# Optimization experiments

Measured on AMD Instinct MI355X. Metric: run time of the kernel, lower is better.

## Reference

```python
import jax, jax.numpy as jnp
import numpy as np

BS, N, F_IN, H, F_OUT = 4, 2048, 128, 4, 64


def setup_inputs() -> dict:
    key = jax.random.key(0)
    k1, k2, k3, k4, k5 = jax.random.split(key, 5)
    x = jax.random.normal(k1, (BS, N, F_IN), dtype=jnp.float32)
    adj = jax.random.randint(k2, (BS, N, N), 0, 2).astype(bool)
    # guarantee self-loops so no softmax row is all -inf
    adj = jnp.logical_or(adj, jnp.eye(N, dtype=bool)[None])
    # xavier-uniform-ish scales
    w = jax.random.uniform(k3, (H, F_IN, F_OUT), dtype=jnp.float32,
                           minval=-1.0, maxval=1.0) * np.sqrt(6.0 / (F_IN + F_OUT))
    a_src = jax.random.uniform(k4, (H, F_OUT, 1), dtype=jnp.float32,
                               minval=-1.0, maxval=1.0) * np.sqrt(6.0 / (F_OUT + 1))
    a_dst = jax.random.uniform(k5, (H, F_OUT, 1), dtype=jnp.float32,
                               minval=-1.0, maxval=1.0) * np.sqrt(6.0 / (F_OUT + 1))
    bias = jnp.zeros((F_OUT,), dtype=jnp.float32)
    return {"x": x, "adj": adj, "w": w, "a_src": a_src, "a_dst": a_dst, "bias": bias}


def reference(x, adj, w, a_src, a_dst, bias):
    bs, n = x.shape[:2]
    # h_prime: [bs, H, n, F_OUT]
    h = jnp.einsum('bnf,hfo->bhno', x, w)
    th = jnp.tanh(h)
    s_src = jnp.einsum('bhno,ho->bhn', th, a_src[..., 0])  # [bs,H,n]
    s_dst = jnp.einsum('bhno,ho->bhn', th, a_dst[..., 0])  # [bs,H,n]
    # attn[b,h,i,j] = src[b,h,i] + dst[b,h,j]
    attn = s_src[..., :, None] + s_dst[..., None, :]
    attn = jnp.where(attn >= 0, attn, 0.2 * attn)  # leaky_relu(0.2)
    attn = jnp.where(adj[:, None], attn, -jnp.inf)  # mask = ~adj
    p = jax.nn.softmax(attn, axis=-1)  # dropout is identity at eval
    out = jnp.einsum('bhij,bhjo->bhio', p, h) + bias  # [bs,H,n,F_OUT]
    # torch .view(bs, n, -1) on contiguous [bs,H,n,F_OUT]: raw reshape
    return out.reshape(bs, n, -1)
```

## Files before the change

kernel.cpp:

```cpp
#include <hip/hip_runtime.h>
#include <hip/hip_fp16.h>

#define NN   2048
#define FIN  128
#define FOUT 64
#define LOG2E 1.44269504088896f

using f16x8 = __attribute__((ext_vector_type(8))) _Float16;
using f16x4 = __attribute__((ext_vector_type(4))) _Float16;
using f16x2 = __attribute__((ext_vector_type(2))) _Float16;
using f32x4 = __attribute__((ext_vector_type(4))) float;
using i32x4 = __attribute__((ext_vector_type(4))) int;

__device__ inline float fast_exp2(float x) {
#if __has_builtin(__builtin_amdgcn_exp2f)
    return __builtin_amdgcn_exp2f(x);
#else
    return exp2f(x);
#endif
}
__device__ inline float fast_rcp(float x) {
#if __has_builtin(__builtin_amdgcn_rcpf)
    return __builtin_amdgcn_rcpf(x);
#else
    return 1.0f / x;
#endif
}
__device__ inline float fast_tanh(float x) {
    float e = fast_exp2(2.0f * LOG2E * x);
    return 1.0f - 2.0f * fast_rcp(e + 1.0f);
}
__device__ inline unsigned cvt2h(float a, float b) {
    return __builtin_bit_cast(unsigned, __builtin_amdgcn_cvt_pkrtz(a, b));
}
__device__ inline f16x2 pkmax(f16x2 a, f16x2 b) {
#if __has_builtin(__builtin_elementwise_max)
    return __builtin_elementwise_max(a, b);
#else
    f16x2 r; r[0] = a[0] > b[0] ? a[0] : b[0]; r[1] = a[1] > b[1] ? a[1] : b[1];
    return r;
#endif
}
__device__ inline unsigned bmask(unsigned wb, int p) {
    unsigned lo = (unsigned)(-(int)((wb >> (2 * p)) & 1u));
    unsigned hi = (unsigned)(-(int)((wb >> (2 * p + 1)) & 1u));
    return (hi & 0xFFFF0000u) | (lo & 0x0000FFFFu);
}


__global__ __launch_bounds__(256) void k1_proj(
    const float* __restrict__ x, const float* __restrict__ w,
    const float* __restrict__ a_src, const float* __restrict__ a_dst,
    const int* __restrict__ adj,
    _Float16* __restrict__ h16B, float* __restrict__ ssrc, float* __restrict__ sdst,
    unsigned int* __restrict__ adjbits)
{
    __shared__ __align__(16) _Float16 xf[8192];
    __shared__ __align__(16) _Float16 wf[8192];

    const int t    = threadIdx.x;
    const int bx   = blockIdx.x;
    const int bh   = bx >> 5;
    const int tile = bx & 31;
    const int b    = bh >> 2;
    const int h    = bh & 3;
    const int n0   = tile * 64;
    const int wv   = t >> 6;
    const int lane = t & 63;
    const int m    = lane & 15;
    const int g    = lane >> 4;

    {
        const int o  = t & 63;
        const int kc = t >> 6;
        const float* wcol = w + h * FIN * FOUT + o;
        _Float16* dst = wf + ((kc * 4 + (o >> 4)) * 512) + (o & 15) * 8;
#pragma unroll
        for (int hi = 0; hi < 4; ++hi) {
            unsigned u0 = cvt2h(wcol[(kc * 32 + hi * 8 + 0) * FOUT],
                                wcol[(kc * 32 + hi * 8 + 1) * FOUT]);
            unsigned u1 = cvt2h(wcol[(kc * 32 + hi * 8 + 2) * FOUT],
                                wcol[(kc * 32 + hi * 8 + 3) * FOUT]);
            unsigned u2 = cvt2h(wcol[(kc * 32 + hi * 8 + 4) * FOUT],
                                wcol[(kc * 32 + hi * 8 + 5) * FOUT]);
            unsigned u3 = cvt2h(wcol[(kc * 32 + hi * 8 + 6) * FOUT],
                                wcol[(kc * 32 + hi * 8 + 7) * FOUT]);
            *(uint4*)(dst + hi * 128) = uint4{u0, u1, u2, u3};
        }
    }
    {
        const int r  = t >> 2;
        const int kc = t & 3;
        const float* xr = x + ((size_t)(b * NN + n0 + r)) * FIN + kc * 32;
        _Float16* dst = xf + ((r >> 4) * 16 + kc * 4) * 128 + (r & 15) * 8;
#pragma unroll
        for (int g2 = 0; g2 < 4; ++g2) {
            f32x4 va = *(const f32x4*)(xr + g2 * 8);
            f32x4 vb = *(const f32x4*)(xr + g2 * 8 + 4);
            *(uint4*)(dst + g2 * 128) = uint4{cvt2h(va[0], va[1]), cvt2h(va[2], va[3]),
                                              cvt2h(vb[0], vb[1]), cvt2h(vb[2], vb[3])};
        }
    }
    __syncthreads();

    const int rg = wv;
    f32x4 acc0 = {0,0,0,0}, acc1 = {0,0,0,0}, acc2 = {0,0,0,0}, acc3 = {0,0,0,0};
#pragma unroll
    for (int kc = 0; kc < 4; ++kc) {
        f16x8 av = *(const f16x8*)(xf + (rg * 16 + kc * 4 + g) * 128 + m * 8);
        const _Float16* wb_ = wf + kc * 4 * 512 + lane * 8;
        acc0 = __builtin_amdgcn_mfma_f32_16x16x32_f16(av, *(const f16x8*)(wb_), acc0, 0, 0, 0);
        acc1 = __builtin_amdgcn_mfma_f32_16x16x32_f16(av, *(const f16x8*)(wb_ + 512), acc1, 0, 0, 0);
        acc2 = __builtin_amdgcn_mfma_f32_16x16x32_f16(av, *(const f16x8*)(wb_ + 1024), acc2, 0, 0, 0);
        acc3 = __builtin_amdgcn_mfma_f32_16x16x32_f16(av, *(const f16x8*)(wb_ + 1536), acc3, 0, 0, 0);
    }

    float s1r[4] = {0,0,0,0}, s2r[4] = {0,0,0,0};
    const int jg = n0 + rg * 16 + g * 4;
#define PROC(accX, ot)  do {                                                    \
        float asv = a_src[h * FOUT + (ot) * 16 + m];                            \
        float adv = a_dst[h * FOUT + (ot) * 16 + m];                            \
        _Pragma("unroll")                                                       \
        for (int r = 0; r < 4; ++r) {                                           \
            float th = fast_tanh(accX[r]);                                      \
            s1r[r] += th * asv;                                                 \
            s2r[r] += th * adv;                                                 \
        }                                                                       \
        unsigned u0 = cvt2h(accX[0], accX[1]);                                  \
        unsigned u1 = cvt2h(accX[2], accX[3]);                                  \
        int off = bh * 131072 + (jg >> 5) * 2048 + (ot) * 512                   \
                + (((jg >> 3) & 3) * 16 + m) * 8 + (jg & 7);                    \
        *(uint2*)(h16B + off) = uint2{u0, u1};                                  \
    } while (0)
    PROC(acc0, 0); PROC(acc1, 1); PROC(acc2, 2); PROC(acc3, 3);
#undef PROC
#pragma unroll
    for (int msk = 1; msk <= 8; msk <<= 1) {
#pragma unroll
        for (int r = 0; r < 4; ++r) {
            s1r[r] += __shfl_xor(s1r[r], msk);
            s2r[r] += __shfl_xor(s2r[r], msk);
        }
    }
    if (m == 0) {
#pragma unroll
        for (int r = 0; r < 4; ++r) {
            ssrc[bh * NN + jg + r] = s1r[r] * LOG2E;
            sdst[bh * NN + jg + r] = s2r[r] * LOG2E;
        }
    }

    {
        const int  frow0 = bx * 16;
        const int* asrc  = adj + (size_t)frow0 * NN;
#pragma unroll
        for (int w4 = 0; w4 < 4; ++w4) {
            int widx  = t + 256 * w4;
            int row_l = widx >> 6;
            int wc    = widx & 63;
            const i32x4* p = (const i32x4*)(asrc + (size_t)row_l * NN + wc * 32);
            unsigned int wbits = 0;
#pragma unroll
            for (int k = 0; k < 8; ++k) {
                i32x4 v = p[k];
                wbits |= (unsigned int)(v[0] & 1) << (4 * k);
                wbits |= (unsigned int)(v[1] & 1) << (4 * k + 1);
                wbits |= (unsigned int)(v[2] & 1) << (4 * k + 2);
                wbits |= (unsigned int)(v[3] & 1) << (4 * k + 3);
            }
            adjbits[(size_t)(frow0 + row_l) * 64 + wc] = wbits;
        }
    }
}

__global__ __launch_bounds__(512, 6) void k2_attn(
    const unsigned int* __restrict__ adjbits,
    const _Float16* __restrict__ h16B,
    const float* __restrict__ ssrc, const float* __restrict__ sdst,
    const float* __restrict__ bias, float* __restrict__ out)
{
    __shared__ __align__(16) char smem[42016];
    _Float16*     Bf     = (_Float16*)smem;
    unsigned int* adjw   = (unsigned int*)(smem + 16384);
    _Float16*     E1h    = (_Float16*)(smem + 33792);
    _Float16*     E2h    = (_Float16*)(smem + 37888);
    float*        redmax = (float*)(smem + 41984);
    float*        comb   = (float*)smem;

    const int t    = threadIdx.x;
    const int wv   = t >> 6;
    const int lane = t & 63;
    const int bh   = blockIdx.x >> 5;
    const int i0   = (blockIdx.x & 31) << 6;
    const int b    = bh >> 2;
    const int rg   = wv >> 1;
    const int par  = wv & 1;
    const int m    = lane & 15;
    const int g    = lane >> 4;

    const _Float16* Bsrc = h16B + bh * 131072;

#define STAGE(bufi_, s_)                                                        \
    __builtin_amdgcn_global_load_lds(                                           \
        (const __attribute__((address_space(1))) unsigned int*)(Bsrc + (s_) * 4096 + t * 8), \
        (__attribute__((address_space(3))) unsigned int*)(Bf + (bufi_) * 4096 + t * 8), \
        16, 0, 0)

    STAGE(0, 0);
    {
        const uint4* asrc = (const uint4*)(adjbits + ((size_t)b * NN + i0) * 64);
#pragma unroll
        for (int k = 0; k < 2; ++k) {
            int idx = t + 512 * k;
            uint4 v = asrc[idx];
            *(uint4*)(adjw + (idx >> 4) * 68 + (idx & 15) * 4) = v;
        }
    }
    float dm;
    {
        f32x4 dv = *(const f32x4*)(sdst + bh * NN + t * 4);
        *(uint2*)(E1h + t * 4) = uint2{cvt2h(fast_exp2(dv[0]), fast_exp2(dv[1])),
                                       cvt2h(fast_exp2(dv[2]), fast_exp2(dv[3]))};
        *(uint2*)(E2h + t * 4) = uint2{cvt2h(fast_exp2(0.2f * dv[0]), fast_exp2(0.2f * dv[1])),
                                       cvt2h(fast_exp2(0.2f * dv[2]), fast_exp2(0.2f * dv[3]))};
        dm = fmaxf(fmaxf(dv[0], dv[1]), fmaxf(dv[2], dv[3]));
#pragma unroll
        for (int msk = 1; msk <= 32; msk <<= 1) dm = fmaxf(dm, __shfl_xor(dm, msk));
        if (lane == 0) redmax[wv] = dm;
    }
    asm volatile("s_waitcnt vmcnt(0)" ::: "memory");
    __syncthreads();

    float D = redmax[0];
#pragma unroll
    for (int k = 1; k < 8; ++k) D = fmaxf(D, redmax[k]);

    const int row = i0 + rg * 16 + m;
    const float sA = ssrc[bh * NN + row];
    float c = sA + D; c = fmaxf(c, 0.2f * c);
    const float K1f = fast_exp2(sA - c);
    const float K2f = fast_exp2(fmaf(0.2f, sA, -c));
    f16x2 K1h2; { _Float16 q = (_Float16)K1f; K1h2[0] = q; K1h2[1] = q; }
    f16x2 K2h2; { _Float16 q = (_Float16)K2f; K2h2[0] = q; K2h2[1] = q; }

    f32x4 acc0 = {0,0,0,0}, acc1 = {0,0,0,0}, acc2 = {0,0,0,0}, acc3 = {0,0,0,0};
    f32x4 accz = {0,0,0,0};
    f16x8 ones;
#pragma unroll
    for (int i = 0; i < 8; ++i) ones[i] = (_Float16)1.0f;

    const int arow68 = (rg * 16 + m) * 68;

#pragma unroll
    for (int s = 0; s < 32; ++s) {
        if (s < 31) {
            STAGE((s + 1) & 1, s + 1);
            asm volatile("s_waitcnt vmcnt(1)" ::: "memory");
        } else {
            asm volatile("s_waitcnt vmcnt(0)" ::: "memory");
        }
        __builtin_amdgcn_sched_barrier(0);
        __builtin_amdgcn_s_barrier();
        __builtin_amdgcn_sched_barrier(0);

        const int ci = 2 * s + par;
        unsigned wb = adjw[arow68 + ci] >> (8 * g);
        union { f16x8 v; f16x2 p[4]; unsigned u[4]; } E1u, E2u, af;
        E1u.v = *(const f16x8*)(E1h + ci * 32 + 8 * g);
        E2u.v = *(const f16x8*)(E2h + ci * 32 + 8 * g);

        const _Float16* bb = Bf + (s & 1) * 4096 + par * 2048 + lane * 8;
        f16x8 b0 = *(const f16x8*)(bb);
        f16x8 b1 = *(const f16x8*)(bb + 512);
        f16x8 b2 = *(const f16x8*)(bb + 1024);
        f16x8 b3 = *(const f16x8*)(bb + 1536);

#pragma unroll
        for (int p = 0; p < 4; ++p) {
            f16x2 v1 = K1h2 * E1u.p[p];
            f16x2 v2 = K2h2 * E2u.p[p];
            f16x2 vm = pkmax(v1, v2);
            af.u[p] = __builtin_bit_cast(unsigned, vm) & bmask(wb, p);
        }

        acc0 = __builtin_amdgcn_mfma_f32_16x16x32_f16(af.v, b0, acc0, 0, 0, 0);
        acc1 = __builtin_amdgcn_mfma_f32_16x16x32_f16(af.v, b1, acc1, 0, 0, 0);
        acc2 = __builtin_amdgcn_mfma_f32_16x16x32_f16(af.v, b2, acc2, 0, 0, 0);
        acc3 = __builtin_amdgcn_mfma_f32_16x16x32_f16(af.v, b3, acc3, 0, 0, 0);
        accz = __builtin_amdgcn_mfma_f32_16x16x32_f16(af.v, ones, accz, 0, 0, 0);

        __builtin_amdgcn_s_barrier();
    }
#undef STAGE

    __syncthreads();
    if (par == 1) {
        float* cp = comb + (rg * 64 + lane) * 20;
#pragma unroll
        for (int r = 0; r < 4; ++r) {
            cp[0 + r]  = acc0[r];
            cp[4 + r]  = acc1[r];
            cp[8 + r]  = acc2[r];
            cp[12 + r] = acc3[r];
            cp[16 + r] = accz[r];
        }
    }
    __syncthreads();
    if (par == 0) {
        const float* cp = comb + (rg * 64 + lane) * 20;
        float zs[4];
#pragma unroll
        for (int r = 0; r < 4; ++r) zs[r] = accz[r] + cp[16 + r];
        size_t obase = ((size_t)bh * NN + i0 + rg * 16) * FOUT;
#pragma unroll
        for (int ot = 0; ot < 4; ++ot) {
            float bv = bias[ot * 16 + m];
            f32x4 a = (ot == 0) ? acc0 : (ot == 1) ? acc1 : (ot == 2) ? acc2 : acc3;
#pragma unroll
            for (int r = 0; r < 4; ++r) {
                float v = (a[r] + cp[ot * 4 + r]) / zs[r] + bv;
                out[obase + (size_t)(g * 4 + r) * FOUT + ot * 16 + m] = v;
            }
        }
    }
}

extern "C" void kernel_launch(void* const* d_in, const int* in_sizes, int n_in,
                              void* d_out, int out_size, void* d_ws, size_t ws_size,
                              hipStream_t stream) {
    (void)in_sizes; (void)n_in; (void)out_size; (void)ws_size;
    const float* x     = (const float*)d_in[0];
    const int*   adj   = (const int*)d_in[1];
    const float* w     = (const float*)d_in[2];
    const float* a_src = (const float*)d_in[3];
    const float* a_dst = (const float*)d_in[4];
    const float* bias  = (const float*)d_in[5];
    float*       out   = (float*)d_out;

    _Float16*     h16B    = (_Float16*)d_ws;
    float*        ssrc    = (float*)((char*)d_ws + 4194304);
    float*        sdst    = (float*)((char*)d_ws + 4194304 + 131072);
    unsigned int* adjbits = (unsigned int*)((char*)d_ws + 4718592);

    k1_proj<<<512, 256, 0, stream>>>(x, w, a_src, a_dst, adj, h16B, ssrc, sdst, adjbits);
    k2_attn<<<512, 512, 0, stream>>>(adjbits, h16B, ssrc, sdst, bias, out);
}
```

Before: 41.31 us.

## Switch attention aggregation to 32x32x16 MFMA with 4-way key split

The attention kernel moves from 16x16x32 MFMA tiles to 32x32x16 tiles: each wave owns 32 query rows and one quarter of each 128-key stage. The h16 layout written by the first kernel is reshuffled to match the new B operand pattern, and stages now hold 128 keys (two LDS loads per thread, 16 iterations). Partial sums are combined with a two-level LDS reduction across the four key quarters. The aim is fewer MFMA issues and less per-key overhead, at the cost of more LDS, lower occupancy (launch bounds 6 to 4) and a heavier epilogue reduction.

```diff
diff --git a/kernel.cpp b/kernel.cpp
--- a/kernel.cpp
+++ b/kernel.cpp
@@ -6,11 +6,12 @@
 #define FOUT 64
 #define LOG2E 1.44269504088896f
 
-using f16x8 = __attribute__((ext_vector_type(8))) _Float16;
-using f16x4 = __attribute__((ext_vector_type(4))) _Float16;
-using f16x2 = __attribute__((ext_vector_type(2))) _Float16;
-using f32x4 = __attribute__((ext_vector_type(4))) float;
-using i32x4 = __attribute__((ext_vector_type(4))) int;
+using f16x8  = __attribute__((ext_vector_type(8))) _Float16;
+using f16x4  = __attribute__((ext_vector_type(4))) _Float16;
+using f16x2  = __attribute__((ext_vector_type(2))) _Float16;
+using f32x4  = __attribute__((ext_vector_type(4))) float;
+using f32x16 = __attribute__((ext_vector_type(16))) float;
+using i32x4  = __attribute__((ext_vector_type(4))) int;
 
 __device__ inline float fast_exp2(float x) {
 #if __has_builtin(__builtin_amdgcn_exp2f)
@@ -128,8 +129,8 @@
         }                                                                       \
         unsigned u0 = cvt2h(accX[0], accX[1]);                                  \
         unsigned u1 = cvt2h(accX[2], accX[3]);                                  \
-        int off = bh * 131072 + (jg >> 5) * 2048 + (ot) * 512                   \
-                + (((jg >> 3) & 3) * 16 + m) * 8 + (jg & 7);                    \
+        int off = bh * 131072 + (jg >> 4) * 1024 + ((ot) >> 1) * 512            \
+                + ((((ot) & 1) * 16 + m) + 32 * ((jg >> 3) & 1)) * 8 + (jg & 7);\
         *(uint2*)(h16B + off) = uint2{u0, u1};                                  \
     } while (0)
     PROC(acc0, 0); PROC(acc1, 1); PROC(acc2, 2); PROC(acc3, 3);
@@ -173,18 +174,18 @@
     }
 }
 
-__global__ __launch_bounds__(512, 6) void k2_attn(
+__global__ __launch_bounds__(512, 4) void k2_attn(
     const unsigned int* __restrict__ adjbits,
     const _Float16* __restrict__ h16B,
     const float* __restrict__ ssrc, const float* __restrict__ sdst,
     const float* __restrict__ bias, float* __restrict__ out)
 {
-    __shared__ __align__(16) char smem[42016];
+    __shared__ __align__(16) char smem[57664];
     _Float16*     Bf     = (_Float16*)smem;
-    unsigned int* adjw   = (unsigned int*)(smem + 16384);
-    _Float16*     E1h    = (_Float16*)(smem + 33792);
-    _Float16*     E2h    = (_Float16*)(smem + 37888);
-    float*        redmax = (float*)(smem + 41984);
+    unsigned int* adjw   = (unsigned int*)(smem + 32768);
+    _Float16*     E1h    = (_Float16*)(smem + 49408);
+    _Float16*     E2h    = (_Float16*)(smem + 53504);
+    float*        redmax = (float*)(smem + 57600);
     float*        comb   = (float*)smem;
 
     const int t    = threadIdx.x;
@@ -193,37 +194,44 @@
     const int bh   = blockIdx.x >> 5;
     const int i0   = (blockIdx.x & 31) << 6;
     const int b    = bh >> 2;
-    const int rg   = wv >> 1;
-    const int par  = wv & 1;
-    const int m    = lane & 15;
-    const int g    = lane >> 4;
+    const int rt   = wv >> 2;
+    const int quad = wv & 3;
+    const int mm   = lane & 31;
+    const int gg   = lane >> 5;
 
     const _Float16* Bsrc = h16B + bh * 131072;
 
-#define STAGE(bufi_, s_)                                                        \
+#define STAGE(bufi_, s_) do {                                                   \
+    const _Float16* gs_ = Bsrc + (s_) * 8192 + t * 8;                           \
+    _Float16*       ld_ = Bf + (bufi_) * 8192 + t * 8;                          \
     __builtin_amdgcn_global_load_lds(                                           \
-        (const __attribute__((address_space(1))) unsigned int*)(Bsrc + (s_) * 4096 + t * 8), \
-        (__attribute__((address_space(3))) unsigned int*)(Bf + (bufi_) * 4096 + t * 8), \
-        16, 0, 0)
+        (const __attribute__((address_space(1))) unsigned int*)gs_,             \
+        (__attribute__((address_space(3))) unsigned int*)ld_, 16, 0, 0);        \
+    __builtin_amdgcn_global_load_lds(                                           \
+        (const __attribute__((address_space(1))) unsigned int*)(gs_ + 4096),    \
+        (__attribute__((address_space(3))) unsigned int*)(ld_ + 4096), 16, 0, 0);\
+    } while (0)
 
     STAGE(0, 0);
     {
         const uint4* asrc = (const uint4*)(adjbits + ((size_t)b * NN + i0) * 64);
 #pragma unroll
         for (int k = 0; k < 2; ++k) {
-            int idx = t + 512 * k;
-            uint4 v = asrc[idx];
-            *(uint4*)(adjw + (idx >> 4) * 68 + (idx & 15) * 4) = v;
-        }
-    }
-    float dm;
+            int u   = t + 512 * k;
+            uint4 v = asrc[u];
+            int row = u >> 4;
+            int wc  = (u & 15) * 4;
+            unsigned int* dst = adjw + row * 65 + wc;
+            dst[0] = v.x; dst[1] = v.y; dst[2] = v.z; dst[3] = v.w;
+        }
+    }
     {
         f32x4 dv = *(const f32x4*)(sdst + bh * NN + t * 4);
         *(uint2*)(E1h + t * 4) = uint2{cvt2h(fast_exp2(dv[0]), fast_exp2(dv[1])),
                                        cvt2h(fast_exp2(dv[2]), fast_exp2(dv[3]))};
         *(uint2*)(E2h + t * 4) = uint2{cvt2h(fast_exp2(0.2f * dv[0]), fast_exp2(0.2f * dv[1])),
                                        cvt2h(fast_exp2(0.2f * dv[2]), fast_exp2(0.2f * dv[3]))};
-        dm = fmaxf(fmaxf(dv[0], dv[1]), fmaxf(dv[2], dv[3]));
+        float dm = fmaxf(fmaxf(dv[0], dv[1]), fmaxf(dv[2], dv[3]));
 #pragma unroll
         for (int msk = 1; msk <= 32; msk <<= 1) dm = fmaxf(dm, __shfl_xor(dm, msk));
         if (lane == 0) redmax[wv] = dm;
@@ -235,7 +243,7 @@
 #pragma unroll
     for (int k = 1; k < 8; ++k) D = fmaxf(D, redmax[k]);
 
-    const int row = i0 + rg * 16 + m;
+    const int row = i0 + rt * 32 + mm;
     const float sA = ssrc[bh * NN + row];
     float c = sA + D; c = fmaxf(c, 0.2f * c);
     const float K1f = fast_exp2(sA - c);
@@ -243,19 +251,18 @@
     f16x2 K1h2; { _Float16 q = (_Float16)K1f; K1h2[0] = q; K1h2[1] = q; }
     f16x2 K2h2; { _Float16 q = (_Float16)K2f; K2h2[0] = q; K2h2[1] = q; }
 
-    f32x4 acc0 = {0,0,0,0}, acc1 = {0,0,0,0}, acc2 = {0,0,0,0}, acc3 = {0,0,0,0};
-    f32x4 accz = {0,0,0,0};
+    f32x16 ac0 = (f32x16)0.0f, ac1 = (f32x16)0.0f, az = (f32x16)0.0f;
     f16x8 ones;
 #pragma unroll
     for (int i = 0; i < 8; ++i) ones[i] = (_Float16)1.0f;
 
-    const int arow68 = (rg * 16 + m) * 68;
-
-#pragma unroll
-    for (int s = 0; s < 32; ++s) {
-        if (s < 31) {
+    const int arow = (rt * 32 + mm) * 65;
+
+#pragma unroll
+    for (int s = 0; s < 16; ++s) {
+        if (s < 15) {
             STAGE((s + 1) & 1, s + 1);
-            asm volatile("s_waitcnt vmcnt(1)" ::: "memory");
+            asm volatile("s_waitcnt vmcnt(2)" ::: "memory");
         } else {
             asm volatile("s_waitcnt vmcnt(0)" ::: "memory");
         }
@@ -263,64 +270,74 @@
         __builtin_amdgcn_s_barrier();
         __builtin_amdgcn_sched_barrier(0);
 
-        const int ci = 2 * s + par;
-        unsigned wb = adjw[arow68 + ci] >> (8 * g);
-        union { f16x8 v; f16x2 p[4]; unsigned u[4]; } E1u, E2u, af;
-        E1u.v = *(const f16x8*)(E1h + ci * 32 + 8 * g);
-        E2u.v = *(const f16x8*)(E2h + ci * 32 + 8 * g);
-
-        const _Float16* bb = Bf + (s & 1) * 4096 + par * 2048 + lane * 8;
-        f16x8 b0 = *(const f16x8*)(bb);
-        f16x8 b1 = *(const f16x8*)(bb + 512);
-        f16x8 b2 = *(const f16x8*)(bb + 1024);
-        f16x8 b3 = *(const f16x8*)(bb + 1536);
-
-#pragma unroll
-        for (int p = 0; p < 4; ++p) {
-            f16x2 v1 = K1h2 * E1u.p[p];
-            f16x2 v2 = K2h2 * E2u.p[p];
-            f16x2 vm = pkmax(v1, v2);
-            af.u[p] = __builtin_bit_cast(unsigned, vm) & bmask(wb, p);
-        }
-
-        acc0 = __builtin_amdgcn_mfma_f32_16x16x32_f16(af.v, b0, acc0, 0, 0, 0);
-        acc1 = __builtin_amdgcn_mfma_f32_16x16x32_f16(af.v, b1, acc1, 0, 0, 0);
-        acc2 = __builtin_amdgcn_mfma_f32_16x16x32_f16(af.v, b2, acc2, 0, 0, 0);
-        acc3 = __builtin_amdgcn_mfma_f32_16x16x32_f16(af.v, b3, acc3, 0, 0, 0);
-        accz = __builtin_amdgcn_mfma_f32_16x16x32_f16(af.v, ones, accz, 0, 0, 0);
+        const unsigned wb = adjw[arow + s * 4 + quad];
+        const int jb = s * 128 + quad * 32;
+        const _Float16* bufb = Bf + (s & 1) * 8192 + (quad * 2) * 1024;
+
+#pragma unroll
+        for (int js = 0; js < 2; ++js) {
+            unsigned w8 = wb >> (js * 16 + 8 * gg);
+            union { f16x8 v; f16x2 p[4]; } E1u, E2u;
+            union { f16x8 v; unsigned u[4]; f16x2 p[4]; } af;
+            E1u.v = *(const f16x8*)(E1h + jb + js * 16 + 8 * gg);
+            E2u.v = *(const f16x8*)(E2h + jb + js * 16 + 8 * gg);
+#pragma unroll
+            for (int p = 0; p < 4; ++p) {
+                f16x2 v1 = K1h2 * E1u.p[p];
+                f16x2 v2 = K2h2 * E2u.p[p];
+                af.u[p] = __builtin_bit_cast(unsigned, pkmax(v1, v2)) & bmask(w8, p);
+            }
+            f16x8 b0 = *(const f16x8*)(bufb + js * 1024 + lane * 8);
+            f16x8 b1 = *(const f16x8*)(bufb + js * 1024 + 512 + lane * 8);
+            ac0 = __builtin_amdgcn_mfma_f32_32x32x16_f16(af.v, b0, ac0, 0, 0, 0);
+            ac1 = __builtin_amdgcn_mfma_f32_32x32x16_f16(af.v, b1, ac1, 0, 0, 0);
+            az  = __builtin_amdgcn_mfma_f32_32x32x16_f16(af.v, ones, az, 0, 0, 0);
+        }
 
         __builtin_amdgcn_s_barrier();
     }
 #undef STAGE
 
     __syncthreads();
-    if (par == 1) {
-        float* cp = comb + (rg * 64 + lane) * 20;
-#pragma unroll
-        for (int r = 0; r < 4; ++r) {
-            cp[0 + r]  = acc0[r];
-            cp[4 + r]  = acc1[r];
-            cp[8 + r]  = acc2[r];
-            cp[12 + r] = acc3[r];
-            cp[16 + r] = accz[r];
-        }
-    }
-    __syncthreads();
-    if (par == 0) {
-        const float* cp = comb + (rg * 64 + lane) * 20;
-        float zs[4];
-#pragma unroll
-        for (int r = 0; r < 4; ++r) zs[r] = accz[r] + cp[16 + r];
-        size_t obase = ((size_t)bh * NN + i0 + rg * 16) * FOUT;
-#pragma unroll
-        for (int ot = 0; ot < 4; ++ot) {
-            float bv = bias[ot * 16 + m];
-            f32x4 a = (ot == 0) ? acc0 : (ot == 1) ? acc1 : (ot == 2) ? acc2 : acc3;
-#pragma unroll
-            for (int r = 0; r < 4; ++r) {
-                float v = (a[r] + cp[ot * 4 + r]) / zs[r] + bv;
-                out[obase + (size_t)(g * 4 + r) * FOUT + ot * 16 + m] = v;
-            }
+    if (quad & 1) {
+        int slot = rt * 2 + (quad >> 1);
+        float* cp = comb + (slot * 64 + lane) * 49;
+#pragma unroll
+        for (int r = 0; r < 16; ++r) {
+            cp[r] = ac0[r]; cp[16 + r] = ac1[r]; cp[32 + r] = az[r];
+        }
+    }
+    __syncthreads();
+    if (!(quad & 1)) {
+        int slot = rt * 2 + (quad >> 1);
+        const float* cp = comb + (slot * 64 + lane) * 49;
+#pragma unroll
+        for (int r = 0; r < 16; ++r) {
+            ac0[r] += cp[r]; ac1[r] += cp[16 + r]; az[r] += cp[32 + r];
+        }
+    }
+    __syncthreads();
+    if (quad == 2) {
+        float* cp = comb + (rt * 64 + lane) * 49;
+#pragma unroll
+        for (int r = 0; r < 16; ++r) {
+            cp[r] = ac0[r]; cp[16 + r] = ac1[r]; cp[32 + r] = az[r];
+        }
+    }
+    __syncthreads();
+    if (quad == 0) {
+        const float* cp = comb + (rt * 64 + lane) * 49;
+        float bv0 = bias[mm];
+        float bv1 = bias[32 + mm];
+        size_t obase = ((size_t)bh * NN + i0 + rt * 32) * FOUT;
+#pragma unroll
+        for (int r = 0; r < 16; ++r) {
+            int rowl = (r & 3) + 8 * (r >> 2) + 4 * gg;
+            float z  = az[r] + cp[32 + r];
+            float v0 = (ac0[r] + cp[r])      / z + bv0;
+            float v1 = (ac1[r] + cp[16 + r]) / z + bv1;
+            out[obase + (size_t)rowl * FOUT + mm]      = v0;
+            out[obase + (size_t)rowl * FOUT + 32 + mm] = v1;
         }
     }
 }
```

After: 43.27 us. +4.7%, slower.

## Process two row groups per wave to reuse staged value tiles

Applied to the files above, without the earlier changes.

Each k2_attn block now covers 128 query rows instead of 64. Every wave computes two 16-row groups against the same staged h tiles and E1/E2 vectors, which halves the total global-to-LDS traffic for h and the per-tile barrier overhead. The grid shrinks from 512 to 256 blocks. Launch bounds drop to 2 blocks per SM and LDS use grows, which lowers occupancy and doubles accumulator registers. Fewer blocks may also leave some CUs idle on a large GPU.

```diff
diff --git a/kernel.cpp b/kernel.cpp
--- a/kernel.cpp
+++ b/kernel.cpp
@@ -173,30 +173,32 @@
     }
 }
 
-__global__ __launch_bounds__(512, 6) void k2_attn(
+__global__ __launch_bounds__(512, 2) void k2_attn(
     const unsigned int* __restrict__ adjbits,
     const _Float16* __restrict__ h16B,
     const float* __restrict__ ssrc, const float* __restrict__ sdst,
     const float* __restrict__ bias, float* __restrict__ out)
 {
-    __shared__ __align__(16) char smem[42016];
+    __shared__ __align__(16) char smem[59424];
     _Float16*     Bf     = (_Float16*)smem;
     unsigned int* adjw   = (unsigned int*)(smem + 16384);
-    _Float16*     E1h    = (_Float16*)(smem + 33792);
-    _Float16*     E2h    = (_Float16*)(smem + 37888);
-    float*        redmax = (float*)(smem + 41984);
+    _Float16*     E1h    = (_Float16*)(smem + 51200);
+    _Float16*     E2h    = (_Float16*)(smem + 55296);
+    float*        redmax = (float*)(smem + 59392);
     float*        comb   = (float*)smem;
 
     const int t    = threadIdx.x;
     const int wv   = t >> 6;
     const int lane = t & 63;
-    const int bh   = blockIdx.x >> 5;
-    const int i0   = (blockIdx.x & 31) << 6;
+    const int bh   = blockIdx.x >> 4;
+    const int i0   = (blockIdx.x & 15) << 7;
     const int b    = bh >> 2;
-    const int rg   = wv >> 1;
+    const int rgp  = wv >> 1;
     const int par  = wv & 1;
     const int m    = lane & 15;
     const int g    = lane >> 4;
+    const int rgA  = rgp * 2;
+    const int rgB  = rgp * 2 + 1;
 
     const _Float16* Bsrc = h16B + bh * 131072;
 
@@ -210,20 +212,19 @@
     {
         const uint4* asrc = (const uint4*)(adjbits + ((size_t)b * NN + i0) * 64);
 #pragma unroll
-        for (int k = 0; k < 2; ++k) {
+        for (int k = 0; k < 4; ++k) {
             int idx = t + 512 * k;
             uint4 v = asrc[idx];
             *(uint4*)(adjw + (idx >> 4) * 68 + (idx & 15) * 4) = v;
         }
     }
-    float dm;
     {
         f32x4 dv = *(const f32x4*)(sdst + bh * NN + t * 4);
         *(uint2*)(E1h + t * 4) = uint2{cvt2h(fast_exp2(dv[0]), fast_exp2(dv[1])),
                                        cvt2h(fast_exp2(dv[2]), fast_exp2(dv[3]))};
         *(uint2*)(E2h + t * 4) = uint2{cvt2h(fast_exp2(0.2f * dv[0]), fast_exp2(0.2f * dv[1])),
                                        cvt2h(fast_exp2(0.2f * dv[2]), fast_exp2(0.2f * dv[3]))};
-        dm = fmaxf(fmaxf(dv[0], dv[1]), fmaxf(dv[2], dv[3]));
+        float dm = fmaxf(fmaxf(dv[0], dv[1]), fmaxf(dv[2], dv[3]));
 #pragma unroll
         for (int msk = 1; msk <= 32; msk <<= 1) dm = fmaxf(dm, __shfl_xor(dm, msk));
         if (lane == 0) redmax[wv] = dm;
@@ -235,21 +236,29 @@
 #pragma unroll
     for (int k = 1; k < 8; ++k) D = fmaxf(D, redmax[k]);
 
-    const int row = i0 + rg * 16 + m;
-    const float sA = ssrc[bh * NN + row];
-    float c = sA + D; c = fmaxf(c, 0.2f * c);
-    const float K1f = fast_exp2(sA - c);
-    const float K2f = fast_exp2(fmaf(0.2f, sA, -c));
-    f16x2 K1h2; { _Float16 q = (_Float16)K1f; K1h2[0] = q; K1h2[1] = q; }
-    f16x2 K2h2; { _Float16 q = (_Float16)K2f; K2h2[0] = q; K2h2[1] = q; }
-
-    f32x4 acc0 = {0,0,0,0}, acc1 = {0,0,0,0}, acc2 = {0,0,0,0}, acc3 = {0,0,0,0};
-    f32x4 accz = {0,0,0,0};
+    const float sA_a = ssrc[bh * NN + i0 + rgA * 16 + m];
+    const float sA_b = ssrc[bh * NN + i0 + rgB * 16 + m];
+    float c_a = sA_a + D; c_a = fmaxf(c_a, 0.2f * c_a);
+    float c_b = sA_b + D; c_b = fmaxf(c_b, 0.2f * c_b);
+    const float K1a = fast_exp2(sA_a - c_a);
+    const float K2a = fast_exp2(fmaf(0.2f, sA_a, -c_a));
+    const float K1b = fast_exp2(sA_b - c_b);
+    const float K2b = fast_exp2(fmaf(0.2f, sA_b, -c_b));
+    f16x2 K1a2, K2a2, K1b2, K2b2;
+    { _Float16 q = (_Float16)K1a; K1a2[0] = q; K1a2[1] = q; }
+    { _Float16 q = (_Float16)K2a; K2a2[0] = q; K2a2[1] = q; }
+    { _Float16 q = (_Float16)K1b; K1b2[0] = q; K1b2[1] = q; }
+    { _Float16 q = (_Float16)K2b; K2b2[0] = q; K2b2[1] = q; }
+
+    f32x4 aA0 = {0,0,0,0}, aA1 = {0,0,0,0}, aA2 = {0,0,0,0}, aA3 = {0,0,0,0};
+    f32x4 aB0 = {0,0,0,0}, aB1 = {0,0,0,0}, aB2 = {0,0,0,0}, aB3 = {0,0,0,0};
+    f32x4 zA = {0,0,0,0}, zB = {0,0,0,0};
     f16x8 ones;
 #pragma unroll
     for (int i = 0; i < 8; ++i) ones[i] = (_Float16)1.0f;
 
-    const int arow68 = (rg * 16 + m) * 68;
+    const int arowA = (rgA * 16 + m) * 68;
+    const int arowB = (rgB * 16 + m) * 68;
 
 #pragma unroll
     for (int s = 0; s < 32; ++s) {
@@ -264,8 +273,9 @@
         __builtin_amdgcn_sched_barrier(0);
 
         const int ci = 2 * s + par;
-        unsigned wb = adjw[arow68 + ci] >> (8 * g);
-        union { f16x8 v; f16x2 p[4]; unsigned u[4]; } E1u, E2u, af;
+        unsigned wbA = adjw[arowA + ci] >> (8 * g);
+        unsigned wbB = adjw[arowB + ci] >> (8 * g);
+        union { f16x8 v; f16x2 p[4]; unsigned u[4]; } E1u, E2u, afA, afB;
         E1u.v = *(const f16x8*)(E1h + ci * 32 + 8 * g);
         E2u.v = *(const f16x8*)(E2h + ci * 32 + 8 * g);
 
@@ -277,17 +287,22 @@
 
 #pragma unroll
         for (int p = 0; p < 4; ++p) {
-            f16x2 v1 = K1h2 * E1u.p[p];
-            f16x2 v2 = K2h2 * E2u.p[p];
-            f16x2 vm = pkmax(v1, v2);
-            af.u[p] = __builtin_bit_cast(unsigned, vm) & bmask(wb, p);
-        }
-
-        acc0 = __builtin_amdgcn_mfma_f32_16x16x32_f16(af.v, b0, acc0, 0, 0, 0);
-        acc1 = __builtin_amdgcn_mfma_f32_16x16x32_f16(af.v, b1, acc1, 0, 0, 0);
-        acc2 = __builtin_amdgcn_mfma_f32_16x16x32_f16(af.v, b2, acc2, 0, 0, 0);
-        acc3 = __builtin_amdgcn_mfma_f32_16x16x32_f16(af.v, b3, acc3, 0, 0, 0);
-        accz = __builtin_amdgcn_mfma_f32_16x16x32_f16(af.v, ones, accz, 0, 0, 0);
+            f16x2 e1 = E1u.p[p];
+            f16x2 e2 = E2u.p[p];
+            afA.u[p] = __builtin_bit_cast(unsigned, pkmax(K1a2 * e1, K2a2 * e2)) & bmask(wbA, p);
+            afB.u[p] = __builtin_bit_cast(unsigned, pkmax(K1b2 * e1, K2b2 * e2)) & bmask(wbB, p);
+        }
+
+        aA0 = __builtin_amdgcn_mfma_f32_16x16x32_f16(afA.v, b0, aA0, 0, 0, 0);
+        aA1 = __builtin_amdgcn_mfma_f32_16x16x32_f16(afA.v, b1, aA1, 0, 0, 0);
+        aA2 = __builtin_amdgcn_mfma_f32_16x16x32_f16(afA.v, b2, aA2, 0, 0, 0);
+        aA3 = __builtin_amdgcn_mfma_f32_16x16x32_f16(afA.v, b3, aA3, 0, 0, 0);
+        zA  = __builtin_amdgcn_mfma_f32_16x16x32_f16(afA.v, ones, zA, 0, 0, 0);
+        aB0 = __builtin_amdgcn_mfma_f32_16x16x32_f16(afB.v, b0, aB0, 0, 0, 0);
+        aB1 = __builtin_amdgcn_mfma_f32_16x16x32_f16(afB.v, b1, aB1, 0, 0, 0);
+        aB2 = __builtin_amdgcn_mfma_f32_16x16x32_f16(afB.v, b2, aB2, 0, 0, 0);
+        aB3 = __builtin_amdgcn_mfma_f32_16x16x32_f16(afB.v, b3, aB3, 0, 0, 0);
+        zB  = __builtin_amdgcn_mfma_f32_16x16x32_f16(afB.v, ones, zB, 0, 0, 0);
 
         __builtin_amdgcn_s_barrier();
     }
@@ -295,31 +310,39 @@
 
     __syncthreads();
     if (par == 1) {
-        float* cp = comb + (rg * 64 + lane) * 20;
+        float* cp = comb + (rgp * 64 + lane) * 41;
 #pragma unroll
         for (int r = 0; r < 4; ++r) {
-            cp[0 + r]  = acc0[r];
-            cp[4 + r]  = acc1[r];
-            cp[8 + r]  = acc2[r];
-            cp[12 + r] = acc3[r];
-            cp[16 + r] = accz[r];
+            cp[0 + r]  = aA0[r]; cp[4 + r]  = aA1[r];
+            cp[8 + r]  = aA2[r]; cp[12 + r] = aA3[r];
+            cp[16 + r] = zA[r];
+            cp[20 + r] = aB0[r]; cp[24 + r] = aB1[r];
+            cp[28 + r] = aB2[r]; cp[32 + r] = aB3[r];
+            cp[36 + r] = zB[r];
         }
     }
     __syncthreads();
     if (par == 0) {
-        const float* cp = comb + (rg * 64 + lane) * 20;
-        float zs[4];
-#pragma unroll
-        for (int r = 0; r < 4; ++r) zs[r] = accz[r] + cp[16 + r];
-        size_t obase = ((size_t)bh * NN + i0 + rg * 16) * FOUT;
+        const float* cp = comb + (rgp * 64 + lane) * 41;
+        float zsA[4], zsB[4];
+#pragma unroll
+        for (int r = 0; r < 4; ++r) {
+            zsA[r] = zA[r] + cp[16 + r];
+            zsB[r] = zB[r] + cp[36 + r];
+        }
+        size_t obaseA = ((size_t)bh * NN + i0 + rgA * 16) * FOUT;
+        size_t obaseB = ((size_t)bh * NN + i0 + rgB * 16) * FOUT;
 #pragma unroll
         for (int ot = 0; ot < 4; ++ot) {
             float bv = bias[ot * 16 + m];
-            f32x4 a = (ot == 0) ? acc0 : (ot == 1) ? acc1 : (ot == 2) ? acc2 : acc3;
+            f32x4 aA = (ot == 0) ? aA0 : (ot == 1) ? aA1 : (ot == 2) ? aA2 : aA3;
+            f32x4 aB = (ot == 0) ? aB0 : (ot == 1) ? aB1 : (ot == 2) ? aB2 : aB3;
 #pragma unroll
             for (int r = 0; r < 4; ++r) {
-                float v = (a[r] + cp[ot * 4 + r]) / zs[r] + bv;
-                out[obase + (size_t)(g * 4 + r) * FOUT + ot * 16 + m] = v;
+                float vA = (aA[r] + cp[ot * 4 + r])      / zsA[r] + bv;
+                float vB = (aB[r] + cp[20 + ot * 4 + r]) / zsB[r] + bv;
+                out[obaseA + (size_t)(g * 4 + r) * FOUT + ot * 16 + m] = vA;
+                out[obaseB + (size_t)(g * 4 + r) * FOUT + ot * 16 + m] = vB;
             }
         }
     }
@@ -343,5 +366,5 @@
     unsigned int* adjbits = (unsigned int*)((char*)d_ws + 4718592);
 
     k1_proj<<<512, 256, 0, stream>>>(x, w, a_src, a_dst, adj, h16B, ssrc, sdst, adjbits);
-    k2_attn<<<512, 512, 0, stream>>>(adjbits, h16B, ssrc, sdst, bias, out);
-}
+    k2_attn<<<256, 512, 0, stream>>>(adjbits, h16B, ssrc, sdst, bias, out);
+}
```

Result: slower. 43.06 us (+4.2%).
